# Optimization experiments

Hardware: AMD Instinct MI355X
Metric: run time of the kernel (lower is better)

Reference implementation:

```python
import jax, jax.numpy as jnp
import numpy as np

C, S, K, SIGMA = 512, 11, 3, 16
B = 128
EPS = 1e-5  # BatchNorm eps (eval mode, running_mean=0, running_var=1)


def _make_dct_weight(Cc, H, W):
    # FcaNet 'low16' frequency selection
    lx = [0, 0, 1, 1, 0, 2, 2, 1, 2, 0, 3, 4, 0, 1, 3, 0]
    ly = [0, 1, 0, 1, 2, 0, 1, 2, 2, 3, 0, 0, 4, 3, 1, 5]
    mx = [u * (H // 7) for u in lx]
    my = [v * (W // 7) for v in ly]
    w = np.zeros((Cc, H, W), np.float32)
    cp = Cc // len(lx)

    def bf(pos, freq, POS):
        r = np.cos(np.pi * freq * (pos + 0.5) / POS) / np.sqrt(POS)
        return r if freq == 0 else r * np.sqrt(2.0)

    for i, (u, v) in enumerate(zip(mx, my)):
        for tx in range(H):
            for ty in range(W):
                w[i * cp:(i + 1) * cp, tx, ty] = bf(tx, u, H) * bf(ty, v, W)
    return jnp.asarray(w)


def _bn(f, g, b):
    # eval-mode BatchNorm2d: (f - 0)/sqrt(1+eps)*g + b, per channel (axis 1)
    s = g / jnp.sqrt(1.0 + EPS)
    return f * s[None, :, None, None] + b[None, :, None, None]


def _conv1x1(f, w, b):
    return jnp.einsum('bchw,oc->bohw', f, w) + b[None, :, None, None]


def _spatial_kernel(f, w_conv, b_conv, g_sp, b_sp):
    Bn = f.shape[0]
    s = _conv1x1(f, w_conv, b_conv)                  # (B, K*K, S, S)
    s = s.reshape(Bn, K * K, S * S).transpose(0, 2, 1)  # (B, S*S, K*K)
    s = _bn(s.reshape(Bn, S * S, K, K), g_sp, b_sp)
    return s.reshape(Bn, S * S, K * K)


def _channel_kernel(f, dct_w, fc1, fc2, g_ch, b_ch):
    y = jnp.sum(f * dct_w[None], axis=(-2, -1))      # (B, C) DCT pooling
    y = jax.nn.sigmoid(jax.nn.relu(y @ fc1.T) @ fc2.T)  # (B, C*K*K)
    y = _bn(y.reshape(-1, C, K, K), g_ch, b_ch)
    return y.reshape(-1, C, K * K)


def _unfold(f):
    # torch-style per-pixel kxk neighborhoods -> (B, C, H, W, K, K)
    p = (K + 1) // 2 - 1
    Bn, Cn, H, W = f.shape
    fp = jnp.pad(f, ((0, 0), (0, 0), (p, p), (p, p)))
    pat = jnp.stack([fp[:, :, di:di + H, dj:dj + W]
                     for di in range(K) for dj in range(K)], axis=-1)
    return pat.reshape(Bn, Cn, H, W, K, K)


def setup_inputs() -> dict:
    key = jax.random.key(0)
    ks = iter(jax.random.split(key, 32))

    def nrm(shape, s=0.02):
        return s * jax.random.normal(next(ks), shape, jnp.float32)

    def gma(shape):
        return 1.0 + 0.1 * jax.random.normal(next(ks), shape, jnp.float32)

    return dict(
        x=jax.random.normal(next(ks), (B, C, S, S), jnp.float32),
        dct_w=_make_dct_weight(C, S, S),
        w_conv=nrm((K * K, C)), b_conv=nrm((K * K,)),
        g_sp=gma((S * S,)), b_sp=nrm((S * S,), 0.05),
        g_ch=gma((C,)), b_ch=nrm((C,), 0.05),
        fc1=nrm((C // SIGMA, C)), fc2=nrm((C * K * K, C // SIGMA)),
        up_w1=nrm((2 * C, C)), up_b1=nrm((2 * C,)), up_g1=gma((2 * C,)), up_bb1=nrm((2 * C,), 0.05),
        up_w2=nrm((2 * C, 2 * C)), up_b2=nrm((2 * C,)), up_g2=gma((2 * C,)), up_bb2=nrm((2 * C,), 0.05),
        lo_w1=nrm((2 * C, 2 * C)), lo_b1=nrm((2 * C,)), lo_g1=gma((2 * C,)), lo_bb1=nrm((2 * C,), 0.05),
        lo_w2=nrm((C, 2 * C)), lo_b2=nrm((C,)), lo_g2=gma((C,)), lo_bb2=nrm((C,), 0.05),
    )


def reference(x, dct_w, w_conv, b_conv, g_sp, b_sp, g_ch, b_ch, fc1, fc2,
              up_w1, up_b1, up_g1, up_bb1, up_w2, up_b2, up_g2, up_bb2,
              lo_w1, lo_b1, lo_g1, lo_bb1, lo_w2, lo_b2, lo_g2, lo_bb2):
    Bn = x.shape[0]
    # instance kernel: spatial (B,1,HW,KK) x channel (B,C,1,KK)
    sk = _spatial_kernel(x, w_conv, b_conv, g_sp, b_sp)[:, None]
    ck = _channel_kernel(x, dct_w, fc1, fc2, g_ch, b_ch)[:, :, None]
    inst = (sk * ck).reshape(Bn, C, S, S, K, K)
    # CLM task representation (sum over batch between upper and lower)
    a = jax.nn.relu(_bn(_conv1x1(x, up_w1, up_b1), up_g1, up_bb1))
    a = jax.nn.relu(_bn(_conv1x1(a, up_w2, up_b2), up_g2, up_bb2))
    a = a.sum(axis=0, keepdims=True)
    a = jax.nn.relu(_bn(_conv1x1(a, lo_w1, lo_b1), lo_g1, lo_bb1))
    task_s = jax.nn.sigmoid(_bn(_conv1x1(a, lo_w2, lo_b2), lo_g2, lo_bb2))
    # task kernel (shared across the batch)
    sk_t = _spatial_kernel(task_s, w_conv, b_conv, g_sp, b_sp)[:, None]
    ck_t = _channel_kernel(task_s, dct_w, fc1, fc2, g_ch, b_ch)[:, :, None]
    task_kernel = (sk_t * ck_t).reshape(1, C, S, S, K, K)
    kernel = task_kernel * inst
    adapted = (_unfold(x) * kernel).mean(axis=(-1, -2))  # (B,C,S,S)
    return adapted + x, task_kernel
```

## Files before the change

kernel.cpp:

```cpp
#include <hip/hip_runtime.h>
#include <hip/hip_bf16.h>
#include <math.h>

#define BNEPS 1e-5f
#define BDIM_B 128
#define CDIM 512
#define SS 121
#define KK 9
#define MROWS (BDIM_B * SS)

typedef unsigned short u16;
typedef __bf16 bf16x8 __attribute__((ext_vector_type(8)));
typedef float f32x4 __attribute__((ext_vector_type(4)));

__device__ __forceinline__ u16 f2bf(float f) {
    union { float f; unsigned int u; } v; v.f = f;
    unsigned int r = v.u + 0x7FFF + ((v.u >> 16) & 1);
    return (u16)(r >> 16);
}
__device__ __forceinline__ float bf2f(u16 v) {
    union { unsigned int u; float f; } x; x.u = ((unsigned int)v) << 16; return x.f;
}

__device__ __forceinline__ void gld16(const u16* g, u16* l) {
    __builtin_amdgcn_global_load_lds(
        (const __attribute__((address_space(1))) void*)g,
        (__attribute__((address_space(3))) void*)l, 16, 0, 0);
}

template<int MODE>
__global__ __launch_bounds__(256)
void gemm_mfma(const u16* __restrict__ A, const u16* __restrict__ Bw,
               const float* __restrict__ bias, const float* __restrict__ g,
               const float* __restrict__ bb, void* __restrict__ out,
               int Kd, int N, int NT)
{
    __shared__ __align__(16) u16 Als[128 * 32];
    __shared__ __align__(16) u16 Bls[128 * 32];

    const int tid  = threadIdx.x;
    const int lane = tid & 63;
    const int w    = tid >> 6;
    const int wm   = w >> 1, wn = w & 1;
    const int lb   = blockIdx.x;
    const int bx   = lb / NT;
    const int by   = lb - bx * NT;
    const int bm   = bx * 128;
    const int bn   = by * 128;

    f32x4 acc[4][4] = {};

    const int subrow = tid >> 2;
    const int kq     = tid & 3;
    const int gchunk = kq ^ ((subrow >> 1) & 3);
    const u16* Ab = A  + (size_t)(bm + subrow) * Kd + gchunk * 8;
    const u16* Bb = Bw + (size_t)(bn + subrow) * Kd + gchunk * 8;
    u16* Al0 = &Als[(w * 16) * 32];
    u16* Al1 = &Als[(w * 16 + 64) * 32];
    u16* Bl0 = &Bls[(w * 16) * 32];
    u16* Bl1 = &Bls[(w * 16 + 64) * 32];

    const int fa_row = wm * 64 + (lane & 15);
    const int fb_row = wn * 64 + (lane & 15);
    const int kofs   = (((lane >> 4) ^ (((lane & 15) >> 1) & 3))) * 8;

    for (int k0 = 0; k0 < Kd; k0 += 32) {
        __syncthreads();
        gld16(Ab + k0, Al0);
        gld16(Ab + (size_t)64 * Kd + k0, Al1);
        gld16(Bb + k0, Bl0);
        gld16(Bb + (size_t)64 * Kd + k0, Bl1);
        __syncthreads();

        bf16x8 af[4], bfv[4];
        #pragma unroll
        for (int i = 0; i < 4; ++i)
            af[i] = *(bf16x8*)&Als[(fa_row + i * 16) * 32 + kofs];
        #pragma unroll
        for (int j = 0; j < 4; ++j)
            bfv[j] = *(bf16x8*)&Bls[(fb_row + j * 16) * 32 + kofs];
        #pragma unroll
        for (int i = 0; i < 4; ++i)
            #pragma unroll
            for (int j = 0; j < 4; ++j)
                acc[i][j] = __builtin_amdgcn_mfma_f32_16x16x32_bf16(af[i], bfv[j], acc[i][j], 0, 0, 0);
    }

    const float inv = 1.0f / sqrtf(1.0f + BNEPS);

    if (MODE == 1) {
        u16* Y = (u16*)out;
        int dstrow[4][4];
        #pragma unroll
        for (int i = 0; i < 4; ++i) {
            int mb = bm + wm * 64 + i * 16 + (lane >> 4) * 4;
            #pragma unroll
            for (int r = 0; r < 4; ++r) {
                int m = mb + r;
                int b = m / 121, p = m - b * 121;
                dstrow[i][r] = p * 128 + b;
            }
        }
        #pragma unroll
        for (int j = 0; j < 4; ++j) {
            int n = bn + wn * 64 + j * 16 + (lane & 15);
            float sc = g[n] * inv, bo = bias[n], bv = bb[n];
            #pragma unroll
            for (int i = 0; i < 4; ++i)
                #pragma unroll
                for (int r = 0; r < 4; ++r) {
                    float v = (acc[i][j][r] + bo) * sc + bv;
                    v = fmaxf(v, 0.0f);
                    Y[(size_t)dstrow[i][r] * N + n] = f2bf(v);
                }
        }
    } else if (MODE == 2) {
        float ps[4];
        #pragma unroll
        for (int j = 0; j < 4; ++j) {
            int n = bn + wn * 64 + j * 16 + (lane & 15);
            float sc = g[n] * inv, bo = bias[n], bv = bb[n];
            float s = 0.f;
            #pragma unroll
            for (int i = 0; i < 4; ++i)
                #pragma unroll
                for (int r = 0; r < 4; ++r) {
                    float v = (acc[i][j][r] + bo) * sc + bv;
                    s += fmaxf(v, 0.0f);
                }
            ps[j] = s;
        }
        __syncthreads();
        float* red = (float*)Als;
        #pragma unroll
        for (int j = 0; j < 4; ++j)
            red[(wm * 4 + (lane >> 4)) * 128 + wn * 64 + j * 16 + (lane & 15)] = ps[j];
        __syncthreads();
        if (tid < 128) {
            float s = 0.f;
            #pragma unroll
            for (int r = 0; r < 8; ++r) s += red[r * 128 + tid];
            ((float*)out)[(size_t)bx * N + bn + tid] = s;
        }
    } else {
        u16* Y = (u16*)out;
        #pragma unroll
        for (int j = 0; j < 4; ++j) {
            int n = bn + wn * 64 + j * 16 + (lane & 15);
            float sc = g[n] * inv, bo = bias[n], bv = bb[n];
            #pragma unroll
            for (int i = 0; i < 4; ++i) {
                int mb = bm + wm * 64 + i * 16 + (lane >> 4) * 4;
                #pragma unroll
                for (int r = 0; r < 4; ++r) {
                    float v = (acc[i][j][r] + bo) * sc + bv;
                    if (MODE == 3) v = fmaxf(v, 0.0f);
                    else           v = 1.f / (1.f + expf(-v));
                    Y[(size_t)(mb + r) * N + n] = f2bf(v);
                }
            }
        }
    }
}

__global__ void transpose_x(const float* __restrict__ x, u16* __restrict__ Xb)
{
    __shared__ float t[64 * 121];
    int b = blockIdx.x, c0 = blockIdx.y * 64;
    for (int idx = threadIdx.x; idx < 64 * 121; idx += 256) {
        int c = idx / 121, p = idx - c * 121;
        t[idx] = x[((size_t)b * 512 + c0 + c) * 121 + p];
    }
    __syncthreads();
    for (int idx = threadIdx.x; idx < 121 * 64; idx += 256) {
        int p = idx >> 6, c = idx & 63;
        Xb[((size_t)(b * 121 + p)) * 512 + c0 + c] = f2bf(t[c * 121 + p]);
    }
}

#define W1N (1024 * 512)
#define W2N (1024 * 1024)
#define L1N (1024 * 1024)
#define L2N (512 * 1024)
__global__ void conv_weights(const float* __restrict__ w1, const float* __restrict__ w2,
                             const float* __restrict__ l1, const float* __restrict__ l2,
                             u16* __restrict__ o1, u16* __restrict__ o2,
                             u16* __restrict__ o3, u16* __restrict__ o4)
{
    int i = blockIdx.x * 256 + threadIdx.x;
    if (i < W1N) { o1[i] = f2bf(w1[i]); return; }
    i -= W1N;
    if (i < W2N) { o2[i] = f2bf(w2[i]); return; }
    i -= W2N;
    if (i < L1N) { o3[i] = f2bf(l1[i]); return; }
    i -= L1N;
    if (i < L2N) { o4[i] = f2bf(l2[i]); }
}

__global__ void f32_to_bf16(const float* __restrict__ in, u16* __restrict__ out, int n)
{
    int i = blockIdx.x * 256 + threadIdx.x;
    if (i < n) out[i] = f2bf(in[i]);
}

__global__ void transpose_dct(const float* __restrict__ dct, float* __restrict__ dctT)
{
    int idx = blockIdx.x * 256 + threadIdx.x;
    if (idx >= 512 * 121) return;
    int p = idx >> 9, c = idx & 511;
    dctT[idx] = dct[(size_t)c * 121 + p];
}

__global__ __launch_bounds__(256)
void rowdot9(const u16* __restrict__ Xb, const u16* __restrict__ Xt,
             const float* __restrict__ w_conv, const float* __restrict__ b_conv,
             const float* __restrict__ g_sp, const float* __restrict__ b_sp,
             float* __restrict__ skb, float* __restrict__ skt)
{
    int wid = (blockIdx.x * 256 + threadIdx.x) >> 6;
    int lane = threadIdx.x & 63;
    if (wid >= MROWS + SS) return;
    const u16* src = (wid < MROWS) ? Xb + (size_t)wid * 512
                                   : Xt + (size_t)(wid - MROWS) * 512;
    bf16x8 xv = *(const bf16x8*)(src + lane * 8);
    float xf[8];
    #pragma unroll
    for (int j = 0; j < 8; ++j) xf[j] = (float)xv[j];

    float s[9];
    #pragma unroll
    for (int k9 = 0; k9 < 9; ++k9) {
        const float* wr = w_conv + k9 * 512 + lane * 8;
        float4 w0 = *(const float4*)wr;
        float4 w1 = *(const float4*)(wr + 4);
        s[k9] = xf[0] * w0.x + xf[1] * w0.y + xf[2] * w0.z + xf[3] * w0.w
              + xf[4] * w1.x + xf[5] * w1.y + xf[6] * w1.z + xf[7] * w1.w;
    }
    #pragma unroll
    for (int off = 1; off < 64; off <<= 1)
        #pragma unroll
        for (int k9 = 0; k9 < 9; ++k9)
            s[k9] += __shfl_xor(s[k9], off);

    if (lane < 9) {
        int p = wid % 121;
        float v = (s[lane] + b_conv[lane]) * (g_sp[p] * (1.0f / sqrtf(1.0f + BNEPS))) + b_sp[p];
        float* dst = (wid < MROWS) ? skb + (size_t)wid * 9 : skt + (size_t)(wid - MROWS) * 9;
        dst[lane] = v;
    }
}

__global__ void dct_pool_xb(const u16* __restrict__ Xb, const u16* __restrict__ Xt,
                            const float* __restrict__ dctT,
                            float* __restrict__ ybuf, float* __restrict__ y_t)
{
    int idx = blockIdx.x * 256 + threadIdx.x;
    if (idx >= 129 * 512) return;
    int g = idx >> 9, c = idx & 511;
    const u16* src = (g < 128) ? Xb + (size_t)g * 121 * 512 + c : Xt + c;
    float s = 0.f;
    for (int p = 0; p < SS; ++p)
        s += bf2f(src[(size_t)p * 512]) * dctT[p * 512 + c];
    if (g < 128) ybuf[idx] = s; else y_t[c] = s;
}

__global__ __launch_bounds__(256)
void fc1_fused(const float* __restrict__ ybuf, const float* __restrict__ y_t,
               const float* __restrict__ fc1, float* __restrict__ y2buf,
               float* __restrict__ y2_t)
{
    __shared__ float Als[512];
    int g = blockIdx.x;
    const float* a = (g < 128) ? ybuf + (size_t)g * 512 : y_t;
    for (int i = threadIdx.x; i < 128; i += 256)
        ((float4*)Als)[i] = ((const float4*)a)[i];
    __syncthreads();
    int o = threadIdx.x >> 3, kp = threadIdx.x & 7;
    const float* w = fc1 + (size_t)o * 512;
    float s = 0.f;
    for (int k = kp * 4; k < 512; k += 32) {
        float4 wv = *(const float4*)(w + k);
        float4 av = *(const float4*)(Als + k);
        s += wv.x * av.x + wv.y * av.y + wv.z * av.z + wv.w * av.w;
    }
    s += __shfl_xor(s, 1);
    s += __shfl_xor(s, 2);
    s += __shfl_xor(s, 4);
    if (kp == 0) {
        float v = fmaxf(s, 0.f);
        if (g < 128) y2buf[(size_t)g * 32 + o] = v; else y2_t[o] = v;
    }
}

__global__ void fc2_ck_fused(const float* __restrict__ y2buf, const float* __restrict__ y2_t,
                             const float* __restrict__ fc2,
                             const float* __restrict__ g_ch, const float* __restrict__ b_ch,
                             float* __restrict__ ckbuf, float* __restrict__ ck_t)
{
    int idx = blockIdx.x * 256 + threadIdx.x;
    if (idx >= 129 * CDIM * KK) return;
    int g = idx / (CDIM * KK), o = idx % (CDIM * KK);
    int c = o / KK;
    const float* yb = (g < 128) ? y2buf + (size_t)g * 32 : y2_t;
    const float* w = fc2 + (size_t)o * 32;
    float s = 0.f;
    #pragma unroll
    for (int k = 0; k < 32; ++k) s += yb[k] * w[k];
    s = 1.f / (1.f + expf(-s));
    s = s * (g_ch[c] * (1.0f / sqrtf(1.0f + BNEPS))) + b_ch[c];
    if (g < 128) ckbuf[idx] = s; else ck_t[o] = s;
}

__global__ void task_kernel_write(const float* __restrict__ sk_t, const float* __restrict__ ck_t,
                                  float* __restrict__ tk)
{
    int idx = blockIdx.x * blockDim.x + threadIdx.x;
    if (idx >= CDIM * SS * KK) return;
    int k9 = idx % KK;
    int pc = idx / KK;
    int p = pc % SS, c = pc / SS;
    tk[idx] = sk_t[p * KK + k9] * ck_t[c * KK + k9];
}

__global__ __launch_bounds__(256)
void final_v2(const float* __restrict__ x, const float* __restrict__ skb,
              const float* __restrict__ sk_t, const float* __restrict__ ckbuf,
              const float* __restrict__ ck_t, float* __restrict__ out0)
{
    __shared__ float PS[SS * KK];
    __shared__ float CS[64 * KK];
    __shared__ float XT[64 * SS];
    const int tid = threadIdx.x;
    const int b = blockIdx.x, c0 = blockIdx.y * 64;

    const float* sp = skb + (size_t)b * SS * KK;
    for (int i = tid; i < SS * KK; i += 256) PS[i] = sp[i] * sk_t[i];
    const float* cp = ckbuf + ((size_t)b * CDIM + c0) * KK;
    const float* tp = ck_t + (size_t)c0 * KK;
    for (int i = tid; i < 64 * KK; i += 256) CS[i] = cp[i] * tp[i];
    const float* xp = x + ((size_t)b * CDIM + c0) * SS;
    for (int i = tid; i < 64 * SS; i += 256) XT[i] = xp[i];
    __syncthreads();

    float* op = out0 + ((size_t)b * CDIM + c0) * SS;
    for (int i = tid; i < 64 * SS; i += 256) {
        int c = i / SS, p = i - c * SS;
        int h = p / 11, w = p - h * 11;
        const float* xc = XT + c * SS;
        const float* ps = PS + p * KK;
        const float* cs = CS + c * KK;
        float acc = 0.f;
        #pragma unroll
        for (int di = 0; di < 3; ++di) {
            int hh = h + di - 1;
            bool hv = (unsigned)hh < 11u;
            #pragma unroll
            for (int dj = 0; dj < 3; ++dj) {
                int ww = w + dj - 1;
                int k = di * 3 + dj;
                float xv = (hv && (unsigned)ww < 11u) ? xc[hh * 11 + ww] : 0.f;
                acc += xv * ps[k] * cs[k];
            }
        }
        op[i] = acc * (1.0f / 9.0f) + xc[p];
    }
}

extern "C" void kernel_launch(void* const* d_in, const int* in_sizes, int n_in,
                              void* d_out, int out_size, void* d_ws, size_t ws_size,
                              hipStream_t stream)
{
    const float* x      = (const float*)d_in[0];
    const float* dct_w  = (const float*)d_in[1];
    const float* w_conv = (const float*)d_in[2];
    const float* b_conv = (const float*)d_in[3];
    const float* g_sp   = (const float*)d_in[4];
    const float* b_sp   = (const float*)d_in[5];
    const float* g_ch   = (const float*)d_in[6];
    const float* b_ch   = (const float*)d_in[7];
    const float* fc1    = (const float*)d_in[8];
    const float* fc2    = (const float*)d_in[9];
    const float* up_w1  = (const float*)d_in[10];
    const float* up_b1  = (const float*)d_in[11];
    const float* up_g1  = (const float*)d_in[12];
    const float* up_bb1 = (const float*)d_in[13];
    const float* up_w2  = (const float*)d_in[14];
    const float* up_b2  = (const float*)d_in[15];
    const float* up_g2  = (const float*)d_in[16];
    const float* up_bb2 = (const float*)d_in[17];
    const float* lo_w1  = (const float*)d_in[18];
    const float* lo_b1  = (const float*)d_in[19];
    const float* lo_g1  = (const float*)d_in[20];
    const float* lo_bb1 = (const float*)d_in[21];
    const float* lo_w2  = (const float*)d_in[22];
    const float* lo_b2  = (const float*)d_in[23];
    const float* lo_g2  = (const float*)d_in[24];
    const float* lo_bb2 = (const float*)d_in[25];

    float* out0 = (float*)d_out;
    float* tk   = out0 + (size_t)BDIM_B * CDIM * SS;

    char* ws = (char*)d_ws;
    size_t off = 0;
    auto alloc = [&](size_t bytes) { void* p = ws + off; off += (bytes + 63) & ~(size_t)63; return p; };
    u16*   Xb      = (u16*)alloc((size_t)MROWS * 512 * 2);
    u16*   Y1      = (u16*)alloc((size_t)MROWS * 1024 * 2);
    u16*   w1b     = (u16*)alloc((size_t)W1N * 2);
    u16*   w2b     = (u16*)alloc((size_t)W2N * 2);
    u16*   lw1b    = (u16*)alloc((size_t)L1N * 2);
    u16*   lw2b    = (u16*)alloc((size_t)L2N * 2);
    float* asum    = (float*)alloc((size_t)128 * 1024 * 4);
    u16*   asum_b  = (u16*)alloc((size_t)128 * 1024 * 2);
    u16*   a3b     = (u16*)alloc((size_t)128 * 1024 * 2);
    u16*   ts_pc   = (u16*)alloc((size_t)128 * 512 * 2);
    float* dctT    = (float*)alloc((size_t)SS * 512 * 4);
    float* ybuf    = (float*)alloc((size_t)BDIM_B * CDIM * 4);
    float* y2buf   = (float*)alloc((size_t)BDIM_B * 32 * 4);
    float* ckbuf   = (float*)alloc((size_t)BDIM_B * CDIM * KK * 4);
    float* skbuf   = (float*)alloc((size_t)BDIM_B * SS * KK * 4);
    float* y_t     = (float*)alloc((size_t)CDIM * 4);
    float* y2_t    = (float*)alloc((size_t)32 * 4);
    float* ck_t    = (float*)alloc((size_t)CDIM * KK * 4);
    float* sk_t    = (float*)alloc((size_t)SS * KK * 4);

    hipLaunchKernelGGL(transpose_x, dim3(BDIM_B, 8), dim3(256), 0, stream, x, Xb);
    hipLaunchKernelGGL(conv_weights, dim3((W1N + W2N + L1N + L2N) / 256), dim3(256), 0, stream,
                       up_w1, up_w2, lo_w1, lo_w2, w1b, w2b, lw1b, lw2b);
    hipLaunchKernelGGL(transpose_dct, dim3((512 * 121 + 255) / 256), dim3(256), 0, stream,
                       dct_w, dctT);

    hipLaunchKernelGGL((gemm_mfma<1>), dim3(121 * 8), dim3(256), 0, stream,
                       Xb, w1b, up_b1, up_g1, up_bb1, (void*)Y1, 512, 1024, 8);
    hipLaunchKernelGGL((gemm_mfma<2>), dim3(121 * 8), dim3(256), 0, stream,
                       Y1, w2b, up_b2, up_g2, up_bb2, (void*)asum, 1024, 1024, 8);

    hipLaunchKernelGGL(f32_to_bf16, dim3((128 * 1024) / 256), dim3(256), 0, stream,
                       asum, asum_b, 128 * 1024);
    hipLaunchKernelGGL((gemm_mfma<3>), dim3(8), dim3(256), 0, stream,
                       asum_b, lw1b, lo_b1, lo_g1, lo_bb1, (void*)a3b, 1024, 1024, 8);
    hipLaunchKernelGGL((gemm_mfma<4>), dim3(4), dim3(256), 0, stream,
                       a3b, lw2b, lo_b2, lo_g2, lo_bb2, (void*)ts_pc, 1024, 512, 4);

    hipLaunchKernelGGL(rowdot9, dim3((MROWS + SS + 3) / 4), dim3(256), 0, stream,
                       Xb, ts_pc, w_conv, b_conv, g_sp, b_sp, skbuf, sk_t);

    hipLaunchKernelGGL(dct_pool_xb, dim3((129 * 512) / 256), dim3(256), 0, stream,
                       Xb, ts_pc, dctT, ybuf, y_t);
    hipLaunchKernelGGL(fc1_fused, dim3(129), dim3(256), 0, stream,
                       ybuf, y_t, fc1, y2buf, y2_t);
    hipLaunchKernelGGL(fc2_ck_fused, dim3((129 * CDIM * KK + 255) / 256), dim3(256), 0, stream,
                       y2buf, y2_t, fc2, g_ch, b_ch, ckbuf, ck_t);

    hipLaunchKernelGGL(task_kernel_write, dim3((CDIM * SS * KK + 255) / 256), dim3(256), 0, stream,
                       sk_t, ck_t, tk);

    hipLaunchKernelGGL(final_v2, dim3(BDIM_B, 8), dim3(256), 0, stream,
                       x, skbuf, sk_t, ckbuf, ck_t, out0);
}
```

Before: 354.3 us.

## Fuse prep and channel-chain kernels, swizzle GEMM block order, emit bf16 sums

Merges the weight conversion and DCT transpose into one prep kernel. It also fuses DCT pooling, fc1 and fc2 into a single per-batch channel_chain kernel. The MODE 2 GEMM now writes bf16 column sums directly, which drops the separate f32-to-bf16 pass. A block-index swizzle groups tiles in the large GEMMs for better L2 reuse of the weights. Fewer launches and less intermediate traffic are traded for a channel chain running on only 129 blocks, with fc2 serialized per block, and a swizzle that is hard-coded to 121x8 tiles.

```diff
diff --git a/kernel.cpp b/kernel.cpp
--- a/kernel.cpp
+++ b/kernel.cpp
@@ -28,7 +28,7 @@
         (__attribute__((address_space(3))) void*)l, 16, 0, 0);
 }
 
-template<int MODE>
+template<int MODE, int SWIZ>
 __global__ __launch_bounds__(256)
 void gemm_mfma(const u16* __restrict__ A, const u16* __restrict__ Bw,
                const float* __restrict__ bias, const float* __restrict__ g,
@@ -42,11 +42,21 @@
     const int lane = tid & 63;
     const int w    = tid >> 6;
     const int wm   = w >> 1, wn = w & 1;
-    const int lb   = blockIdx.x;
-    const int bx   = lb / NT;
-    const int by   = lb - bx * NT;
-    const int bm   = bx * 128;
-    const int bn   = by * 128;
+
+    int bx, by;
+    if (SWIZ) {
+        int i = blockIdx.x;
+        if (i < 960) {
+            int xg = i & 7;
+            int j  = i >> 3;
+            bx = xg * 15 + (j >> 3);
+            by = j & 7;
+        } else { bx = 120; by = i - 960; }
+    } else {
+        bx = blockIdx.x / NT; by = blockIdx.x - bx * NT;
+    }
+    const int bm = bx * 128;
+    const int bn = by * 128;
 
     f32x4 acc[4][4] = {};
 
@@ -140,7 +150,7 @@
             float s = 0.f;
             #pragma unroll
             for (int r = 0; r < 8; ++r) s += red[r * 128 + tid];
-            ((float*)out)[(size_t)bx * N + bn + tid] = s;
+            ((u16*)out)[(size_t)bx * N + bn + tid] = f2bf(s);
         }
     } else {
         u16* Y = (u16*)out;
@@ -182,10 +192,13 @@
 #define W2N (1024 * 1024)
 #define L1N (1024 * 1024)
 #define L2N (512 * 1024)
-__global__ void conv_weights(const float* __restrict__ w1, const float* __restrict__ w2,
-                             const float* __restrict__ l1, const float* __restrict__ l2,
-                             u16* __restrict__ o1, u16* __restrict__ o2,
-                             u16* __restrict__ o3, u16* __restrict__ o4)
+#define DCTN (512 * 121)
+__global__ void prep_all(const float* __restrict__ w1, const float* __restrict__ w2,
+                         const float* __restrict__ l1, const float* __restrict__ l2,
+                         const float* __restrict__ dct,
+                         u16* __restrict__ o1, u16* __restrict__ o2,
+                         u16* __restrict__ o3, u16* __restrict__ o4,
+                         float* __restrict__ dctT)
 {
     int i = blockIdx.x * 256 + threadIdx.x;
     if (i < W1N) { o1[i] = f2bf(w1[i]); return; }
@@ -194,21 +207,12 @@
     i -= W2N;
     if (i < L1N) { o3[i] = f2bf(l1[i]); return; }
     i -= L1N;
-    if (i < L2N) { o4[i] = f2bf(l2[i]); }
-}
-
-__global__ void f32_to_bf16(const float* __restrict__ in, u16* __restrict__ out, int n)
-{
-    int i = blockIdx.x * 256 + threadIdx.x;
-    if (i < n) out[i] = f2bf(in[i]);
-}
-
-__global__ void transpose_dct(const float* __restrict__ dct, float* __restrict__ dctT)
-{
-    int idx = blockIdx.x * 256 + threadIdx.x;
-    if (idx >= 512 * 121) return;
-    int p = idx >> 9, c = idx & 511;
-    dctT[idx] = dct[(size_t)c * 121 + p];
+    if (i < L2N) { o4[i] = f2bf(l2[i]); return; }
+    i -= L2N;
+    if (i < DCTN) {
+        int p = i >> 9, c = i & 511;
+        dctT[i] = dct[(size_t)c * 121 + p];
+    }
 }
 
 __global__ __launch_bounds__(256)
@@ -250,65 +254,54 @@
     }
 }
 
-__global__ void dct_pool_xb(const u16* __restrict__ Xb, const u16* __restrict__ Xt,
-                            const float* __restrict__ dctT,
-                            float* __restrict__ ybuf, float* __restrict__ y_t)
-{
-    int idx = blockIdx.x * 256 + threadIdx.x;
-    if (idx >= 129 * 512) return;
-    int g = idx >> 9, c = idx & 511;
-    const u16* src = (g < 128) ? Xb + (size_t)g * 121 * 512 + c : Xt + c;
-    float s = 0.f;
-    for (int p = 0; p < SS; ++p)
-        s += bf2f(src[(size_t)p * 512]) * dctT[p * 512 + c];
-    if (g < 128) ybuf[idx] = s; else y_t[c] = s;
-}
-
 __global__ __launch_bounds__(256)
-void fc1_fused(const float* __restrict__ ybuf, const float* __restrict__ y_t,
-               const float* __restrict__ fc1, float* __restrict__ y2buf,
-               float* __restrict__ y2_t)
-{
-    __shared__ float Als[512];
-    int g = blockIdx.x;
-    const float* a = (g < 128) ? ybuf + (size_t)g * 512 : y_t;
-    for (int i = threadIdx.x; i < 128; i += 256)
-        ((float4*)Als)[i] = ((const float4*)a)[i];
+void channel_chain(const u16* __restrict__ Xb, const u16* __restrict__ Xt,
+                   const float* __restrict__ dctT,
+                   const float* __restrict__ fc1, const float* __restrict__ fc2,
+                   const float* __restrict__ g_ch, const float* __restrict__ b_ch,
+                   float* __restrict__ ckbuf, float* __restrict__ ck_t)
+{
+    __shared__ float yls[512];
+    __shared__ float y2ls[32];
+    const int g = blockIdx.x;
+    const u16* src = (g < 128) ? Xb + (size_t)g * 121 * 512 : Xt;
+
+    for (int c = threadIdx.x; c < 512; c += 256) {
+        float s = 0.f;
+        for (int p = 0; p < SS; ++p)
+            s += bf2f(src[(size_t)p * 512 + c]) * dctT[p * 512 + c];
+        yls[c] = s;
+    }
     __syncthreads();
-    int o = threadIdx.x >> 3, kp = threadIdx.x & 7;
-    const float* w = fc1 + (size_t)o * 512;
-    float s = 0.f;
-    for (int k = kp * 4; k < 512; k += 32) {
-        float4 wv = *(const float4*)(w + k);
-        float4 av = *(const float4*)(Als + k);
-        s += wv.x * av.x + wv.y * av.y + wv.z * av.z + wv.w * av.w;
-    }
-    s += __shfl_xor(s, 1);
-    s += __shfl_xor(s, 2);
-    s += __shfl_xor(s, 4);
-    if (kp == 0) {
-        float v = fmaxf(s, 0.f);
-        if (g < 128) y2buf[(size_t)g * 32 + o] = v; else y2_t[o] = v;
-    }
-}
-
-__global__ void fc2_ck_fused(const float* __restrict__ y2buf, const float* __restrict__ y2_t,
-                             const float* __restrict__ fc2,
-                             const float* __restrict__ g_ch, const float* __restrict__ b_ch,
-                             float* __restrict__ ckbuf, float* __restrict__ ck_t)
-{
-    int idx = blockIdx.x * 256 + threadIdx.x;
-    if (idx >= 129 * CDIM * KK) return;
-    int g = idx / (CDIM * KK), o = idx % (CDIM * KK);
-    int c = o / KK;
-    const float* yb = (g < 128) ? y2buf + (size_t)g * 32 : y2_t;
-    const float* w = fc2 + (size_t)o * 32;
-    float s = 0.f;
-    #pragma unroll
-    for (int k = 0; k < 32; ++k) s += yb[k] * w[k];
-    s = 1.f / (1.f + expf(-s));
-    s = s * (g_ch[c] * (1.0f / sqrtf(1.0f + BNEPS))) + b_ch[c];
-    if (g < 128) ckbuf[idx] = s; else ck_t[o] = s;
+
+    {
+        int o = threadIdx.x >> 3, kp = threadIdx.x & 7;
+        const float* w = fc1 + (size_t)o * 512;
+        float s = 0.f;
+        for (int k = kp * 4; k < 512; k += 32) {
+            float4 wv = *(const float4*)(w + k);
+            float4 av = *(const float4*)(yls + k);
+            s += wv.x * av.x + wv.y * av.y + wv.z * av.z + wv.w * av.w;
+        }
+        s += __shfl_xor(s, 1);
+        s += __shfl_xor(s, 2);
+        s += __shfl_xor(s, 4);
+        if (kp == 0) y2ls[o] = fmaxf(s, 0.f);
+    }
+    __syncthreads();
+
+    const float inv = 1.0f / sqrtf(1.0f + BNEPS);
+    for (int o = threadIdx.x; o < CDIM * KK; o += 256) {
+        const float* w = fc2 + (size_t)o * 32;
+        float s = 0.f;
+        #pragma unroll
+        for (int k = 0; k < 32; ++k) s += y2ls[k] * w[k];
+        s = 1.f / (1.f + expf(-s));
+        int c = o / KK;
+        s = s * (g_ch[c] * inv) + b_ch[c];
+        if (g < 128) ckbuf[(size_t)g * CDIM * KK + o] = s;
+        else         ck_t[o] = s;
+    }
 }
 
 __global__ void task_kernel_write(const float* __restrict__ sk_t, const float* __restrict__ ck_t,
@@ -409,47 +402,34 @@
     u16*   w2b     = (u16*)alloc((size_t)W2N * 2);
     u16*   lw1b    = (u16*)alloc((size_t)L1N * 2);
     u16*   lw2b    = (u16*)alloc((size_t)L2N * 2);
-    float* asum    = (float*)alloc((size_t)128 * 1024 * 4);
     u16*   asum_b  = (u16*)alloc((size_t)128 * 1024 * 2);
     u16*   a3b     = (u16*)alloc((size_t)128 * 1024 * 2);
     u16*   ts_pc   = (u16*)alloc((size_t)128 * 512 * 2);
     float* dctT    = (float*)alloc((size_t)SS * 512 * 4);
-    float* ybuf    = (float*)alloc((size_t)BDIM_B * CDIM * 4);
-    float* y2buf   = (float*)alloc((size_t)BDIM_B * 32 * 4);
     float* ckbuf   = (float*)alloc((size_t)BDIM_B * CDIM * KK * 4);
     float* skbuf   = (float*)alloc((size_t)BDIM_B * SS * KK * 4);
-    float* y_t     = (float*)alloc((size_t)CDIM * 4);
-    float* y2_t    = (float*)alloc((size_t)32 * 4);
     float* ck_t    = (float*)alloc((size_t)CDIM * KK * 4);
     float* sk_t    = (float*)alloc((size_t)SS * KK * 4);
 
     hipLaunchKernelGGL(transpose_x, dim3(BDIM_B, 8), dim3(256), 0, stream, x, Xb);
-    hipLaunchKernelGGL(conv_weights, dim3((W1N + W2N + L1N + L2N) / 256), dim3(256), 0, stream,
-                       up_w1, up_w2, lo_w1, lo_w2, w1b, w2b, lw1b, lw2b);
-    hipLaunchKernelGGL(transpose_dct, dim3((512 * 121 + 255) / 256), dim3(256), 0, stream,
-                       dct_w, dctT);
-
-    hipLaunchKernelGGL((gemm_mfma<1>), dim3(121 * 8), dim3(256), 0, stream,
+    hipLaunchKernelGGL(prep_all, dim3((W1N + W2N + L1N + L2N + DCTN + 255) / 256), dim3(256), 0, stream,
+                       up_w1, up_w2, lo_w1, lo_w2, dct_w, w1b, w2b, lw1b, lw2b, dctT);
+
+    hipLaunchKernelGGL((gemm_mfma<1, 1>), dim3(121 * 8), dim3(256), 0, stream,
                        Xb, w1b, up_b1, up_g1, up_bb1, (void*)Y1, 512, 1024, 8);
-    hipLaunchKernelGGL((gemm_mfma<2>), dim3(121 * 8), dim3(256), 0, stream,
-                       Y1, w2b, up_b2, up_g2, up_bb2, (void*)asum, 1024, 1024, 8);
-
-    hipLaunchKernelGGL(f32_to_bf16, dim3((128 * 1024) / 256), dim3(256), 0, stream,
-                       asum, asum_b, 128 * 1024);
-    hipLaunchKernelGGL((gemm_mfma<3>), dim3(8), dim3(256), 0, stream,
+    hipLaunchKernelGGL((gemm_mfma<2, 1>), dim3(121 * 8), dim3(256), 0, stream,
+                       Y1, w2b, up_b2, up_g2, up_bb2, (void*)asum_b, 1024, 1024, 8);
+
+    hipLaunchKernelGGL((gemm_mfma<3, 0>), dim3(8), dim3(256), 0, stream,
                        asum_b, lw1b, lo_b1, lo_g1, lo_bb1, (void*)a3b, 1024, 1024, 8);
-    hipLaunchKernelGGL((gemm_mfma<4>), dim3(4), dim3(256), 0, stream,
+    hipLaunchKernelGGL((gemm_mfma<4, 0>), dim3(4), dim3(256), 0, stream,
                        a3b, lw2b, lo_b2, lo_g2, lo_bb2, (void*)ts_pc, 1024, 512, 4);
 
     hipLaunchKernelGGL(rowdot9, dim3((MROWS + SS + 3) / 4), dim3(256), 0, stream,
                        Xb, ts_pc, w_conv, b_conv, g_sp, b_sp, skbuf, sk_t);
 
-    hipLaunchKernelGGL(dct_pool_xb, dim3((129 * 512) / 256), dim3(256), 0, stream,
-                       Xb, ts_pc, dctT, ybuf, y_t);
-    hipLaunchKernelGGL(fc1_fused, dim3(129), dim3(256), 0, stream,
-                       ybuf, y_t, fc1, y2buf, y2_t);
-    hipLaunchKernelGGL(fc2_ck_fused, dim3((129 * CDIM * KK + 255) / 256), dim3(256), 0, stream,
-                       y2buf, y2_t, fc2, g_ch, b_ch, ckbuf, ck_t);
+    hipLaunchKernelGGL(channel_chain, dim3(129), dim3(256), 0, stream,
+                       Xb, ts_pc, dctT, fc1, fc2, g_ch, b_ch, ckbuf, ck_t);
 
     hipLaunchKernelGGL(task_kernel_write, dim3((CDIM * SS * KK + 255) / 256), dim3(256), 0, stream,
                        sk_t, ck_t, tk);
```

Result: no change. 351.7 us (-0.7%).
